# Kernel optimization log

Hardware: AMD Instinct MI355X
Metric: run time of the kernel (lower is better)

Reference implementation:

```python
import jax, jax.numpy as jnp
import numpy as np

B, N, E, H = 16, 512, 512, 8
D = E // H
NEG = -1e9  # stands in for -inf; other scores are clamped to [-10, 10]


def setup_inputs() -> dict:
    key = jax.random.key(0)
    ks = jax.random.split(key, 11)
    s = 1.0 / np.sqrt(E)
    return {
        "x": jax.random.normal(ks[0], (B, N, E), jnp.float32),
        "db": jax.random.normal(ks[1], (B, N, N), jnp.float32),
        "mask": jax.random.randint(ks[2], (B, N), 0, 2, jnp.int32),
        "wq": jax.random.normal(ks[3], (E, E), jnp.float32) * s,
        "bq": jax.random.normal(ks[4], (E,), jnp.float32) * s,
        "wk": jax.random.normal(ks[5], (E, E), jnp.float32) * s,
        "bk": jax.random.normal(ks[6], (E,), jnp.float32) * s,
        "wv": jax.random.normal(ks[7], (E, E), jnp.float32) * s,
        "bv": jax.random.normal(ks[8], (E,), jnp.float32) * s,
        "wo": jax.random.normal(ks[9], (E, E), jnp.float32) * s,
        "bo": jax.random.normal(ks[10], (E,), jnp.float32) * s,
    }


def reference(x, db, mask, wq, bq, wk, bk, wv, bv, wo, bo):
    # projections -> [B, H, N, D]
    def proj(w, b):
        return (x @ w.T + b).reshape(B, N, H, D).transpose(0, 2, 1, 3)

    q = proj(wq, bq)
    k = proj(wk, bk)
    v = proj(wv, bv)

    scale = 1.0 / np.sqrt(D).astype(np.float32)
    sc = jnp.einsum('bhid,bhjd->bhij', q, k) * scale + db[:, None, :, :]
    sc = jnp.clip(sc, -10.0, 10.0)
    sc = jnp.where(mask[:, None, None, :].astype(bool), sc, NEG)
    a = jax.nn.softmax(sc, axis=-1)  # dropout is identity (p=0 / eval)
    o = jnp.einsum('bhij,bhjd->bhid', a, v)
    o = o.transpose(0, 2, 1, 3).reshape(B, N, E)
    return o @ wo.T + bo
```

## Files before the change

kernel.cpp:

```cpp
#include <hip/hip_runtime.h>

typedef __attribute__((ext_vector_type(8))) short short8;
typedef __attribute__((ext_vector_type(4))) short short4v;
typedef __attribute__((ext_vector_type(4))) float f32x4;

#define MFMA16(A, B, C) __builtin_amdgcn_mfma_f32_16x16x32_bf16(A, B, C, 0, 0, 0)

__device__ __forceinline__ short f2bf(float f) {
    union { float f; unsigned u; } v;
    v.f = f;
    unsigned r = (v.u + 0x7FFFu + ((v.u >> 16) & 1u)) >> 16;
    return (short)r;
}

__device__ __forceinline__ float bf2f(short u) {
    union { unsigned u; float f; } v;
    v.u = ((unsigned)(unsigned short)u) << 16;
    return v.f;
}

__global__ __launch_bounds__(256) void cvt_all(
    const float* __restrict__ x, const float* __restrict__ wq,
    const float* __restrict__ wk, const float* __restrict__ wv,
    const float* __restrict__ wo, const float* __restrict__ db,
    const int* __restrict__ mask, short* __restrict__ xb,
    short* __restrict__ wcat, short* __restrict__ wob,
    short* __restrict__ dbp) {
    const int blk = blockIdx.x;
    if (blk < 2560) {
        int i = blk * 256 + threadIdx.x;
        const float* src;
        short* dst;
        int soff, doff;
        if (i < 524288) {
            src = x; dst = xb; soff = i; doff = i;
        } else {
            int j = i - 524288;
            int w = j >> 15;
            soff = j & 32767;
            src = (w == 0) ? wq : (w == 1) ? wk : (w == 2) ? wv : wo;
            if (w < 3) { dst = wcat; doff = j; }
            else       { dst = wob;  doff = soff; }
        }
        const float* p = src + (size_t)soff * 8;
        short8 r;
#pragma unroll
        for (int t = 0; t < 8; ++t) r[t] = f2bf(p[t]);
        *(short8*)(dst + (size_t)doff * 8) = r;
    } else {
        int t = (blk - 2560) * 256 + threadIdx.x;
        int f = t * 8;
        int b = f >> 18;
        int rem = f & 262143;
        int qt = rem >> 13;
        int rem2 = rem & 8191;
        int jidx = rem2 >> 10;
        int w = rem2 & 1023;
        int lane = w >> 4;
        int idx0 = w & 15;
        int c = lane & 15, g = lane >> 4;
        int q = qt * 16 + c;
        const float* dbrow = db + ((size_t)b * 512 + q) * 512;
        const int* mrow = mask + b * 512;
        short8 out;
#pragma unroll
        for (int e = 0; e < 8; ++e) {
            int idx = idx0 + e;
            int nt = idx >> 2, r = idx & 3;
            int j = jidx * 64 + nt * 16 + g * 4 + r;
            float val = (mrow[j] != 0) ? dbrow[j] : -1e9f;
            out[e] = f2bf(val);
        }
        *(short8*)(dbp + (size_t)f) = out;
    }
}

__global__ __launch_bounds__(256) void qkv128(
    const short* __restrict__ A, const short* __restrict__ Bw,
    const float* __restrict__ bq, const float* __restrict__ bk,
    const float* __restrict__ bv, short* __restrict__ qo,
    short* __restrict__ ko, short* __restrict__ vto) {
    __shared__ short As[128 * 72];
    __shared__ short Bs[128 * 72];
    const int tid = threadIdx.x, lane = tid & 63, wid = tid >> 6;
    const int c = lane & 15, g = lane >> 4;
    const int wr = (wid >> 1) * 64, wc = (wid & 1) * 64;
    const int m0 = blockIdx.x * 128, e0 = blockIdx.y * 128;

    const f32x4 Z = {0.f, 0.f, 0.f, 0.f};
    f32x4 acc[4][4];
#pragma unroll
    for (int i = 0; i < 4; ++i)
#pragma unroll
        for (int j = 0; j < 4; ++j) acc[i][j] = Z;

    short8 pa[4], pb[4];
#pragma unroll
    for (int p = 0; p < 4; ++p) {
        int u = p * 256 + tid;
        int row = u >> 3, c8 = u & 7;
        pa[p] = *(const short8*)&A[(size_t)(m0 + row) * 512 + c8 * 8];
        pb[p] = *(const short8*)&Bw[(size_t)(e0 + row) * 512 + c8 * 8];
    }
    for (int it = 0; it < 8; ++it) {
        __syncthreads();
#pragma unroll
        for (int p = 0; p < 4; ++p) {
            int u = p * 256 + tid;
            int row = u >> 3, c8 = u & 7;
            *(short8*)&As[row * 72 + c8 * 8] = pa[p];
            *(short8*)&Bs[row * 72 + c8 * 8] = pb[p];
        }
        if (it < 7) {
            int k0 = (it + 1) * 64;
#pragma unroll
            for (int p = 0; p < 4; ++p) {
                int u = p * 256 + tid;
                int row = u >> 3, c8 = u & 7;
                pa[p] = *(const short8*)&A[(size_t)(m0 + row) * 512 + k0 + c8 * 8];
                pb[p] = *(const short8*)&Bw[(size_t)(e0 + row) * 512 + k0 + c8 * 8];
            }
        }
        __syncthreads();
#pragma unroll
        for (int ks = 0; ks < 2; ++ks) {
            short8 af[4], bf[4];
#pragma unroll
            for (int mt = 0; mt < 4; ++mt)
                af[mt] = *(const short8*)&As[(wr + mt * 16 + c) * 72 + ks * 32 + g * 8];
#pragma unroll
            for (int nt = 0; nt < 4; ++nt)
                bf[nt] = *(const short8*)&Bs[(wc + nt * 16 + c) * 72 + ks * 32 + g * 8];
#pragma unroll
            for (int mt = 0; mt < 4; ++mt)
#pragma unroll
                for (int nt = 0; nt < 4; ++nt)
                    acc[mt][nt] = MFMA16(af[mt], bf[nt], acc[mt][nt]);
        }
    }

    const int z = e0 >> 9;
    const float* bp = (z == 0) ? bq : (z == 1) ? bk : bv;
    if (z < 2) {
        short* out = (z == 0) ? qo : ko;
#pragma unroll
        for (int nt = 0; nt < 4; ++nt) {
            int eh = (e0 & 511) + wc + nt * 16 + c;
            float bsv = bp[eh];
            int h = eh >> 6, d = eh & 63;
#pragma unroll
            for (int mt = 0; mt < 4; ++mt)
#pragma unroll
                for (int r = 0; r < 4; ++r) {
                    int m = m0 + wr + mt * 16 + g * 4 + r;
                    int bb = m >> 9, n = m & 511;
                    out[(((size_t)bb * 8 + h) * 512 + n) * 64 + d] =
                        f2bf(acc[mt][nt][r] + bsv);
                }
        }
    } else {
#pragma unroll
        for (int nt = 0; nt < 4; ++nt) {
            int eh = (e0 & 511) + wc + nt * 16 + c;
            float bsv = bp[eh];
            int h = eh >> 6, d = eh & 63;
#pragma unroll
            for (int mt = 0; mt < 4; ++mt) {
                int m = m0 + wr + mt * 16 + g * 4;
                int bb = m >> 9, n = m & 511;
                short4v w;
#pragma unroll
                for (int r = 0; r < 4; ++r) w[r] = f2bf(acc[mt][nt][r] + bsv);
                *(short4v*)&vto[(((size_t)bb * 8 + h) * 64 + d) * 512 + n] = w;
            }
        }
    }
}

__global__ __launch_bounds__(256) void out_gemm(const short* __restrict__ A,
                                                const short* __restrict__ W,
                                                const float* __restrict__ bo,
                                                float* __restrict__ out) {
    __shared__ short As[64 * 72];
    __shared__ short Bs[64 * 72];
    const int tid = threadIdx.x, lane = tid & 63, wid = tid >> 6;
    const int c = lane & 15, g = lane >> 4;
    const int wr = (wid >> 1) * 32, wc = (wid & 1) * 32;
    const int m0 = blockIdx.x * 64, e0 = blockIdx.y * 64;

    const f32x4 Z = {0.f, 0.f, 0.f, 0.f};
    f32x4 acc[2][2];
#pragma unroll
    for (int i = 0; i < 2; ++i)
#pragma unroll
        for (int j = 0; j < 2; ++j) acc[i][j] = Z;

    short8 pa[2], pb[2];
#pragma unroll
    for (int p = 0; p < 2; ++p) {
        int s = p * 256 + tid;
        int row = s >> 3, c8 = s & 7;
        pa[p] = *(const short8*)&A[(size_t)(m0 + row) * 512 + c8 * 8];
        pb[p] = *(const short8*)&W[(size_t)(e0 + row) * 512 + c8 * 8];
    }
    for (int it = 0; it < 8; ++it) {
        __syncthreads();
#pragma unroll
        for (int p = 0; p < 2; ++p) {
            int s = p * 256 + tid;
            int row = s >> 3, c8 = s & 7;
            *(short8*)&As[row * 72 + c8 * 8] = pa[p];
            *(short8*)&Bs[row * 72 + c8 * 8] = pb[p];
        }
        if (it < 7) {
            int k0 = (it + 1) * 64;
#pragma unroll
            for (int p = 0; p < 2; ++p) {
                int s = p * 256 + tid;
                int row = s >> 3, c8 = s & 7;
                pa[p] = *(const short8*)&A[(size_t)(m0 + row) * 512 + k0 + c8 * 8];
                pb[p] = *(const short8*)&W[(size_t)(e0 + row) * 512 + k0 + c8 * 8];
            }
        }
        __syncthreads();
#pragma unroll
        for (int ks = 0; ks < 2; ++ks) {
            short8 af[2], bf[2];
#pragma unroll
            for (int mt = 0; mt < 2; ++mt)
                af[mt] = *(const short8*)&As[(wr + mt * 16 + c) * 72 + ks * 32 + g * 8];
#pragma unroll
            for (int nt = 0; nt < 2; ++nt)
                bf[nt] = *(const short8*)&Bs[(wc + nt * 16 + c) * 72 + ks * 32 + g * 8];
#pragma unroll
            for (int mt = 0; mt < 2; ++mt)
#pragma unroll
                for (int nt = 0; nt < 2; ++nt)
                    acc[mt][nt] = MFMA16(af[mt], bf[nt], acc[mt][nt]);
        }
    }

#pragma unroll
    for (int nt = 0; nt < 2; ++nt) {
        int e = e0 + wc + nt * 16 + c;
        float bsv = bo[e];
#pragma unroll
        for (int mt = 0; mt < 2; ++mt)
#pragma unroll
            for (int r = 0; r < 4; ++r) {
                int m = m0 + wr + mt * 16 + g * 4 + r;
                out[(size_t)m * 512 + e] = acc[mt][nt][r] + bsv;
            }
    }
}

__global__ __launch_bounds__(256, 2) void attn_mfma(
    const short* __restrict__ q, const short* __restrict__ k,
    const short* __restrict__ vt, const short* __restrict__ dbp_all,
    short* __restrict__ o) {
    __shared__ __align__(16) char smem[18432 + 1024];
    short* pl_base = (short*)smem;
    float* ostage = (float*)smem;
    float* lstage = (float*)(smem + 18432);

    const int tid = threadIdx.x;
    const int lane = tid & 63, wid = tid >> 6;
    const int c = lane & 15, g = lane >> 4;
    const int unit = wid >> 1;
    const int jhalf = wid & 1;
    const int f = blockIdx.x;
    const int blo = f & 7;
    const int t = f >> 3;
    const int g2 = t & 7;
    const int h = (t >> 3) & 7;
    const int b = (t >> 6) * 8 + blo;
    const int u = g2 * 2 + unit;
    const int q0A = u * 32;
    const int jstart = jhalf * 256;

    const short* kp = k + (((size_t)b * 8 + h) * 512) * 64;
    const short* vp = vt + (((size_t)b * 8 + h) * 64) * 512;
    const short* qpA = q + (((size_t)b * 8 + h) * 512 + q0A) * 64;
    const short* dbpA = dbp_all + (((size_t)b * 32 + u * 2) * 8 + jhalf * 4) * 1024
                        + lane * 16;
    const short* dbpB = dbpA + 8192;

    short8 qA0 = *(const short8*)&qpA[c * 64 + g * 8];
    short8 qA1 = *(const short8*)&qpA[c * 64 + 32 + g * 8];
    short8 qB0 = *(const short8*)&qpA[(16 + c) * 64 + g * 8];
    short8 qB1 = *(const short8*)&qpA[(16 + c) * 64 + 32 + g * 8];

    short8 kf0[4], kf1[4];
#pragma unroll
    for (int nt = 0; nt < 4; ++nt) {
        kf0[nt] = *(const short8*)&kp[(jstart + nt * 16 + c) * 64 + g * 8];
        kf1[nt] = *(const short8*)&kp[(jstart + nt * 16 + c) * 64 + 32 + g * 8];
    }
    short8 dA0 = *(const short8*)&dbpA[0];
    short8 dA1 = *(const short8*)&dbpA[8];
    short8 dB0 = *(const short8*)&dbpB[0];
    short8 dB1 = *(const short8*)&dbpB[8];

    const f32x4 Z = {0.f, 0.f, 0.f, 0.f};
    f32x4 oA[4], oB[4];
    float lsA[4], lsB[4];
#pragma unroll
    for (int dt = 0; dt < 4; ++dt) { oA[dt] = Z; oB[dt] = Z; }
#pragma unroll
    for (int nt = 0; nt < 4; ++nt) { lsA[nt] = 0.f; lsB[nt] = 0.f; }

    short* plA = pl_base + (wid * 2) * (16 * 72);
    short* plB = plA + 16 * 72;

    for (int jj = 0; jj < 4; ++jj) {
        const int j0 = jstart + jj * 64;
        f32x4 sA[4], sB[4];
        __builtin_amdgcn_s_setprio(1);
#pragma unroll
        for (int nt = 0; nt < 4; ++nt) {
            f32x4 zA = Z, zB = Z;
            zA = MFMA16(kf0[nt], qA0, zA);
            zB = MFMA16(kf0[nt], qB0, zB);
            zA = MFMA16(kf1[nt], qA1, zA);
            zB = MFMA16(kf1[nt], qB1, zB);
            sA[nt] = zA;
            sB[nt] = zB;
        }
        __builtin_amdgcn_s_setprio(0);
        if (jj < 3) {
#pragma unroll
            for (int nt = 0; nt < 4; ++nt) {
                kf0[nt] = *(const short8*)&kp[(j0 + 64 + nt * 16 + c) * 64 + g * 8];
                kf1[nt] = *(const short8*)&kp[(j0 + 64 + nt * 16 + c) * 64 + 32 + g * 8];
            }
        }
        short8 vf0[4], vf1[4];
#pragma unroll
        for (int dt = 0; dt < 4; ++dt) {
            vf0[dt] = *(const short8*)&vp[(dt * 16 + c) * 512 + j0 + g * 8];
            vf1[dt] = *(const short8*)&vp[(dt * 16 + c) * 512 + j0 + 32 + g * 8];
        }
#pragma unroll
        for (int nt = 0; nt < 4; ++nt) {
            short4v w;
            float ps0 = 0.f, ps1 = 0.f;
#pragma unroll
            for (int r = 0; r < 4; ++r) {
                int idx = nt * 4 + r;
                float dv = bf2f(idx < 8 ? dA0[idx] : dA1[idx - 8]);
                float v = fminf(fmaxf(fmaf(sA[nt][r], 0.125f, dv), -10.f), 10.f);
                float pp = exp2f(fmaf(v, 1.442695041f, -14.42695041f));
                w[r] = f2bf(pp);
                if (r < 2) ps0 += pp; else ps1 += pp;
            }
            lsA[nt] += ps0 + ps1;
            *(short4v*)&plA[c * 72 + nt * 16 + g * 4] = w;
        }
        if (jj < 3) {
            dA0 = *(const short8*)&dbpA[(jj + 1) * 1024];
            dA1 = *(const short8*)&dbpA[(jj + 1) * 1024 + 8];
        }
#pragma unroll
        for (int nt = 0; nt < 4; ++nt) {
            short4v w;
            float ps0 = 0.f, ps1 = 0.f;
#pragma unroll
            for (int r = 0; r < 4; ++r) {
                int idx = nt * 4 + r;
                float dv = bf2f(idx < 8 ? dB0[idx] : dB1[idx - 8]);
                float v = fminf(fmaxf(fmaf(sB[nt][r], 0.125f, dv), -10.f), 10.f);
                float pp = exp2f(fmaf(v, 1.442695041f, -14.42695041f));
                w[r] = f2bf(pp);
                if (r < 2) ps0 += pp; else ps1 += pp;
            }
            lsB[nt] += ps0 + ps1;
            *(short4v*)&plB[c * 72 + nt * 16 + g * 4] = w;
        }
        if (jj < 3) {
            dB0 = *(const short8*)&dbpB[(jj + 1) * 1024];
            dB1 = *(const short8*)&dbpB[(jj + 1) * 1024 + 8];
        }
        asm volatile("s_waitcnt lgkmcnt(0)" ::: "memory");
        __builtin_amdgcn_sched_barrier(0);
        short8 pA0 = *(const short8*)&plA[c * 72 + g * 8];
        short8 pA1 = *(const short8*)&plA[c * 72 + 32 + g * 8];
        short8 pB0 = *(const short8*)&plB[c * 72 + g * 8];
        short8 pB1 = *(const short8*)&plB[c * 72 + 32 + g * 8];
        __builtin_amdgcn_s_setprio(1);
#pragma unroll
        for (int dt = 0; dt < 4; ++dt) {
            oA[dt] = MFMA16(vf0[dt], pA0, oA[dt]);
            oB[dt] = MFMA16(vf0[dt], pB0, oB[dt]);
            oA[dt] = MFMA16(vf1[dt], pA1, oA[dt]);
            oB[dt] = MFMA16(vf1[dt], pB1, oB[dt]);
        }
        __builtin_amdgcn_s_setprio(0);
    }

    float lAp = (lsA[0] + lsA[1]) + (lsA[2] + lsA[3]);
    float lBp = (lsB[0] + lsB[1]) + (lsB[2] + lsB[3]);
    __syncthreads();
    if (jhalf == 1) {
#pragma unroll
        for (int dt = 0; dt < 4; ++dt) {
            *(f32x4*)&ostage[((unit * 8 + dt) * 64 + lane) * 4] = oA[dt];
            *(f32x4*)&ostage[((unit * 8 + 4 + dt) * 64 + lane) * 4] = oB[dt];
        }
        lstage[(unit * 64 + lane) * 2] = lAp;
        lstage[(unit * 64 + lane) * 2 + 1] = lBp;
    }
    __syncthreads();
    if (jhalf == 0) {
#pragma unroll
        for (int dt = 0; dt < 4; ++dt) {
            oA[dt] += *(const f32x4*)&ostage[((unit * 8 + dt) * 64 + lane) * 4];
            oB[dt] += *(const f32x4*)&ostage[((unit * 8 + 4 + dt) * 64 + lane) * 4];
        }
        lAp += lstage[(unit * 64 + lane) * 2];
        lBp += lstage[(unit * 64 + lane) * 2 + 1];
        lAp += __shfl_xor(lAp, 16);
        lAp += __shfl_xor(lAp, 32);
        lBp += __shfl_xor(lBp, 16);
        lBp += __shfl_xor(lBp, 32);
        const float invA = 1.f / lAp, invB = 1.f / lBp;
#pragma unroll
        for (int dt = 0; dt < 4; ++dt) {
            short4v wa, wb;
#pragma unroll
            for (int r = 0; r < 4; ++r) {
                wa[r] = f2bf(oA[dt][r] * invA);
                wb[r] = f2bf(oB[dt][r] * invB);
            }
            *(short4v*)&o[((size_t)b * 512 + q0A + c) * 512 + h * 64 + dt * 16 + g * 4] = wa;
            *(short4v*)&o[((size_t)b * 512 + q0A + 16 + c) * 512 + h * 64 + dt * 16 + g * 4] = wb;
        }
    }
}

extern "C" void kernel_launch(void* const* d_in, const int* in_sizes, int n_in,
                              void* d_out, int out_size, void* d_ws, size_t ws_size,
                              hipStream_t stream) {
    const float* x  = (const float*)d_in[0];
    const float* db = (const float*)d_in[1];
    const int* msk  = (const int*)d_in[2];
    const float* wq = (const float*)d_in[3];
    const float* bq = (const float*)d_in[4];
    const float* wk = (const float*)d_in[5];
    const float* bk = (const float*)d_in[6];
    const float* wv = (const float*)d_in[7];
    const float* bv = (const float*)d_in[8];
    const float* wo = (const float*)d_in[9];
    const float* bo = (const float*)d_in[10];
    float* out = (float*)d_out;

    short* xb   = (short*)d_ws;
    short* wcat = xb + 4194304;
    short* wob  = wcat + 786432;
    short* qb   = wob + 262144;
    short* kb   = qb + 4194304;
    short* vtb  = kb + 4194304;
    short* ob   = vtb + 4194304;
    short* dbp  = ob + 4194304;

    cvt_all<<<4608, 256, 0, stream>>>(x, wq, wk, wv, wo, db, msk,
                                      xb, wcat, wob, dbp);
    qkv128<<<dim3(64, 12), 256, 0, stream>>>(xb, wcat, bq, bk, bv, qb, kb, vtb);
    attn_mfma<<<1024, 256, 0, stream>>>(qb, kb, vtb, dbp, ob);
    out_gemm<<<dim3(128, 8), 256, 0, stream>>>(ob, wob, bo, out);
}
```

Before: 88.90 us.

## Keep softmax probabilities in registers via K16 MFMA, drop LDS staging and split-K

The P·V product now uses the 16x16x16 bf16 MFMA, whose B-operand layout matches the accumulator layout of the QK^T MFMA. This lets the exponentiated scores feed the next MFMA straight from registers instead of round-tripping through LDS. Each wave now covers the full 512-key range, which removes the two-wave split over keys, the LDS reduction and both block barriers, and halves the grid to 512 blocks. The cost is twice as many (smaller) MFMAs for P·V, narrower 8-byte V loads, a longer serial loop per wave, and fewer waves available to hide latency.

```diff
diff --git a/kernel.cpp b/kernel.cpp
--- a/kernel.cpp
+++ b/kernel.cpp
@@ -5,6 +5,20 @@
 typedef __attribute__((ext_vector_type(4))) float f32x4;
 
 #define MFMA16(A, B, C) __builtin_amdgcn_mfma_f32_16x16x32_bf16(A, B, C, 0, 0, 0)
+
+#if __has_builtin(__builtin_amdgcn_mfma_f32_16x16x16bf16_1k)
+#define MFMA16K16(A, B, C) __builtin_amdgcn_mfma_f32_16x16x16bf16_1k(A, B, C, 0, 0, 0)
+#elif __has_builtin(__builtin_amdgcn_mfma_f32_16x16x16_bf16)
+#define MFMA16K16(A, B, C) __builtin_amdgcn_mfma_f32_16x16x16_bf16(A, B, C, 0, 0, 0)
+#else
+__device__ __forceinline__ f32x4 mfma16k16_fn(short4v a, short4v b, f32x4 c) {
+    f32x4 d;
+    asm("v_mfma_f32_16x16x16_bf16 %0, %1, %2, %3"
+        : "=v"(d) : "v"(a), "v"(b), "v"(c));
+    return d;
+}
+#define MFMA16K16(A, B, C) mfma16k16_fn(A, B, C)
+#endif
 
 __device__ __forceinline__ short f2bf(float f) {
     union { float f; unsigned u; } v;
@@ -258,31 +272,22 @@
     const short* __restrict__ q, const short* __restrict__ k,
     const short* __restrict__ vt, const short* __restrict__ dbp_all,
     short* __restrict__ o) {
-    __shared__ __align__(16) char smem[18432 + 1024];
-    short* pl_base = (short*)smem;
-    float* ostage = (float*)smem;
-    float* lstage = (float*)(smem + 18432);
-
     const int tid = threadIdx.x;
     const int lane = tid & 63, wid = tid >> 6;
     const int c = lane & 15, g = lane >> 4;
-    const int unit = wid >> 1;
-    const int jhalf = wid & 1;
     const int f = blockIdx.x;
     const int blo = f & 7;
     const int t = f >> 3;
-    const int g2 = t & 7;
-    const int h = (t >> 3) & 7;
-    const int b = (t >> 6) * 8 + blo;
-    const int u = g2 * 2 + unit;
+    const int u4 = t & 3;
+    const int h = (t >> 2) & 7;
+    const int b = (t >> 5) * 8 + blo;
+    const int u = u4 * 4 + wid;
     const int q0A = u * 32;
-    const int jstart = jhalf * 256;
 
     const short* kp = k + (((size_t)b * 8 + h) * 512) * 64;
     const short* vp = vt + (((size_t)b * 8 + h) * 64) * 512;
     const short* qpA = q + (((size_t)b * 8 + h) * 512 + q0A) * 64;
-    const short* dbpA = dbp_all + (((size_t)b * 32 + u * 2) * 8 + jhalf * 4) * 1024
-                        + lane * 16;
+    const short* dbpA = dbp_all + (((size_t)b * 32 + u * 2) * 8) * 1024 + lane * 16;
     const short* dbpB = dbpA + 8192;
 
     short8 qA0 = *(const short8*)&qpA[c * 64 + g * 8];
@@ -293,8 +298,8 @@
     short8 kf0[4], kf1[4];
 #pragma unroll
     for (int nt = 0; nt < 4; ++nt) {
-        kf0[nt] = *(const short8*)&kp[(jstart + nt * 16 + c) * 64 + g * 8];
-        kf1[nt] = *(const short8*)&kp[(jstart + nt * 16 + c) * 64 + 32 + g * 8];
+        kf0[nt] = *(const short8*)&kp[(nt * 16 + c) * 64 + g * 8];
+        kf1[nt] = *(const short8*)&kp[(nt * 16 + c) * 64 + 32 + g * 8];
     }
     short8 dA0 = *(const short8*)&dbpA[0];
     short8 dA1 = *(const short8*)&dbpA[8];
@@ -309,11 +314,8 @@
 #pragma unroll
     for (int nt = 0; nt < 4; ++nt) { lsA[nt] = 0.f; lsB[nt] = 0.f; }
 
-    short* plA = pl_base + (wid * 2) * (16 * 72);
-    short* plB = plA + 16 * 72;
-
-    for (int jj = 0; jj < 4; ++jj) {
-        const int j0 = jstart + jj * 64;
+    for (int jidx = 0; jidx < 8; ++jidx) {
+        const int j0 = jidx * 64;
         f32x4 sA[4], sB[4];
         __builtin_amdgcn_s_setprio(1);
 #pragma unroll
@@ -327,19 +329,20 @@
             sB[nt] = zB;
         }
         __builtin_amdgcn_s_setprio(0);
-        if (jj < 3) {
+        if (jidx < 7) {
 #pragma unroll
             for (int nt = 0; nt < 4; ++nt) {
                 kf0[nt] = *(const short8*)&kp[(j0 + 64 + nt * 16 + c) * 64 + g * 8];
                 kf1[nt] = *(const short8*)&kp[(j0 + 64 + nt * 16 + c) * 64 + 32 + g * 8];
             }
         }
-        short8 vf0[4], vf1[4];
-#pragma unroll
-        for (int dt = 0; dt < 4; ++dt) {
-            vf0[dt] = *(const short8*)&vp[(dt * 16 + c) * 512 + j0 + g * 8];
-            vf1[dt] = *(const short8*)&vp[(dt * 16 + c) * 512 + j0 + 32 + g * 8];
-        }
+        short4v vf[4][4];
+#pragma unroll
+        for (int dt = 0; dt < 4; ++dt)
+#pragma unroll
+            for (int nt = 0; nt < 4; ++nt)
+                vf[dt][nt] = *(const short4v*)&vp[(dt * 16 + c) * 512 + j0 + nt * 16 + g * 4];
+        short4v paf[4], pbf[4];
 #pragma unroll
         for (int nt = 0; nt < 4; ++nt) {
             short4v w;
@@ -354,11 +357,11 @@
                 if (r < 2) ps0 += pp; else ps1 += pp;
             }
             lsA[nt] += ps0 + ps1;
-            *(short4v*)&plA[c * 72 + nt * 16 + g * 4] = w;
-        }
-        if (jj < 3) {
-            dA0 = *(const short8*)&dbpA[(jj + 1) * 1024];
-            dA1 = *(const short8*)&dbpA[(jj + 1) * 1024 + 8];
+            paf[nt] = w;
+        }
+        if (jidx < 7) {
+            dA0 = *(const short8*)&dbpA[(jidx + 1) * 1024];
+            dA1 = *(const short8*)&dbpA[(jidx + 1) * 1024 + 8];
         }
 #pragma unroll
         for (int nt = 0; nt < 4; ++nt) {
@@ -374,66 +377,39 @@
                 if (r < 2) ps0 += pp; else ps1 += pp;
             }
             lsB[nt] += ps0 + ps1;
-            *(short4v*)&plB[c * 72 + nt * 16 + g * 4] = w;
-        }
-        if (jj < 3) {
-            dB0 = *(const short8*)&dbpB[(jj + 1) * 1024];
-            dB1 = *(const short8*)&dbpB[(jj + 1) * 1024 + 8];
-        }
-        asm volatile("s_waitcnt lgkmcnt(0)" ::: "memory");
-        __builtin_amdgcn_sched_barrier(0);
-        short8 pA0 = *(const short8*)&plA[c * 72 + g * 8];
-        short8 pA1 = *(const short8*)&plA[c * 72 + 32 + g * 8];
-        short8 pB0 = *(const short8*)&plB[c * 72 + g * 8];
-        short8 pB1 = *(const short8*)&plB[c * 72 + 32 + g * 8];
+            pbf[nt] = w;
+        }
+        if (jidx < 7) {
+            dB0 = *(const short8*)&dbpB[(jidx + 1) * 1024];
+            dB1 = *(const short8*)&dbpB[(jidx + 1) * 1024 + 8];
+        }
         __builtin_amdgcn_s_setprio(1);
 #pragma unroll
-        for (int dt = 0; dt < 4; ++dt) {
-            oA[dt] = MFMA16(vf0[dt], pA0, oA[dt]);
-            oB[dt] = MFMA16(vf0[dt], pB0, oB[dt]);
-            oA[dt] = MFMA16(vf1[dt], pA1, oA[dt]);
-            oB[dt] = MFMA16(vf1[dt], pB1, oB[dt]);
-        }
+        for (int dt = 0; dt < 4; ++dt)
+#pragma unroll
+            for (int nt = 0; nt < 4; ++nt) {
+                oA[dt] = MFMA16K16(vf[dt][nt], paf[nt], oA[dt]);
+                oB[dt] = MFMA16K16(vf[dt][nt], pbf[nt], oB[dt]);
+            }
         __builtin_amdgcn_s_setprio(0);
     }
-
-    float lAp = (lsA[0] + lsA[1]) + (lsA[2] + lsA[3]);
-    float lBp = (lsB[0] + lsB[1]) + (lsB[2] + lsB[3]);
-    __syncthreads();
-    if (jhalf == 1) {
-#pragma unroll
-        for (int dt = 0; dt < 4; ++dt) {
-            *(f32x4*)&ostage[((unit * 8 + dt) * 64 + lane) * 4] = oA[dt];
-            *(f32x4*)&ostage[((unit * 8 + 4 + dt) * 64 + lane) * 4] = oB[dt];
-        }
-        lstage[(unit * 64 + lane) * 2] = lAp;
-        lstage[(unit * 64 + lane) * 2 + 1] = lBp;
-    }
-    __syncthreads();
-    if (jhalf == 0) {
-#pragma unroll
-        for (int dt = 0; dt < 4; ++dt) {
-            oA[dt] += *(const f32x4*)&ostage[((unit * 8 + dt) * 64 + lane) * 4];
-            oB[dt] += *(const f32x4*)&ostage[((unit * 8 + 4 + dt) * 64 + lane) * 4];
-        }
-        lAp += lstage[(unit * 64 + lane) * 2];
-        lBp += lstage[(unit * 64 + lane) * 2 + 1];
-        lAp += __shfl_xor(lAp, 16);
-        lAp += __shfl_xor(lAp, 32);
-        lBp += __shfl_xor(lBp, 16);
-        lBp += __shfl_xor(lBp, 32);
-        const float invA = 1.f / lAp, invB = 1.f / lBp;
-#pragma unroll
-        for (int dt = 0; dt < 4; ++dt) {
-            short4v wa, wb;
-#pragma unroll
-            for (int r = 0; r < 4; ++r) {
-                wa[r] = f2bf(oA[dt][r] * invA);
-                wb[r] = f2bf(oB[dt][r] * invB);
-            }
-            *(short4v*)&o[((size_t)b * 512 + q0A + c) * 512 + h * 64 + dt * 16 + g * 4] = wa;
-            *(short4v*)&o[((size_t)b * 512 + q0A + 16 + c) * 512 + h * 64 + dt * 16 + g * 4] = wb;
-        }
+    float lA = (lsA[0] + lsA[1]) + (lsA[2] + lsA[3]);
+    lA += __shfl_xor(lA, 16);
+    lA += __shfl_xor(lA, 32);
+    float lB = (lsB[0] + lsB[1]) + (lsB[2] + lsB[3]);
+    lB += __shfl_xor(lB, 16);
+    lB += __shfl_xor(lB, 32);
+    const float invA = 1.f / lA, invB = 1.f / lB;
+#pragma unroll
+    for (int dt = 0; dt < 4; ++dt) {
+        short4v wa, wb;
+#pragma unroll
+        for (int r = 0; r < 4; ++r) {
+            wa[r] = f2bf(oA[dt][r] * invA);
+            wb[r] = f2bf(oB[dt][r] * invB);
+        }
+        *(short4v*)&o[((size_t)b * 512 + q0A + c) * 512 + h * 64 + dt * 16 + g * 4] = wa;
+        *(short4v*)&o[((size_t)b * 512 + q0A + 16 + c) * 512 + h * 64 + dt * 16 + g * 4] = wb;
     }
 }
 
@@ -465,6 +441,6 @@
     cvt_all<<<4608, 256, 0, stream>>>(x, wq, wk, wv, wo, db, msk,
                                       xb, wcat, wob, dbp);
     qkv128<<<dim3(64, 12), 256, 0, stream>>>(xb, wcat, bq, bk, bv, qb, kb, vtb);
-    attn_mfma<<<1024, 256, 0, stream>>>(qb, kb, vtb, dbp, ob);
+    attn_mfma<<<512, 256, 0, stream>>>(qb, kb, vtb, dbp, ob);
     out_gemm<<<dim3(128, 8), 256, 0, stream>>>(ob, wob, bo, out);
 }
```

Measured after the change: 100.1 us. 1.13x slower.
